# Kernel tuning notes

Hardware: AMD Instinct MI355X
Metric: run time of the kernel (lower is better)

The kernel has to match this reference:

```python
import jax, jax.numpy as jnp
import numpy as np

HEAD_DIM = 64
EMBED_DIM = 1024


def setup_inputs() -> dict:
    key = jax.random.key(0)
    k0, k1, k2, k3, k4, k5, k6 = jax.random.split(key, 7)
    B, T = 4, 2048
    s = 1.0 / np.sqrt(EMBED_DIM)
    return {
        "inputs": jax.random.normal(k0, (B, T, EMBED_DIM), dtype=jnp.float32),
        "Wq": jax.random.uniform(k1, (HEAD_DIM, EMBED_DIM), jnp.float32, -s, s),
        "bq": jax.random.uniform(k2, (HEAD_DIM,), jnp.float32, -s, s),
        "Wk": jax.random.uniform(k3, (HEAD_DIM, EMBED_DIM), jnp.float32, -s, s),
        "bk": jax.random.uniform(k4, (HEAD_DIM,), jnp.float32, -s, s),
        "Wv": jax.random.uniform(k5, (HEAD_DIM, EMBED_DIM), jnp.float32, -s, s),
        "bv": jax.random.uniform(k6, (HEAD_DIM,), jnp.float32, -s, s),
    }


def reference(inputs, Wq, bq, Wk, bk, Wv, bv):
    # inputs: [B, T, E]
    q = jnp.einsum("bte,he->bth", inputs, Wq) + bq  # [B, T, H]
    k = jnp.einsum("bte,he->bth", inputs, Wk) + bk
    v = jnp.einsum("bte,he->bth", inputs, Wv) + bv
    scores = jnp.einsum("bth,bsh->bts", q, k)  # [B, T, T]
    T = scores.shape[-1]
    causal = jnp.tril(jnp.ones((T, T), dtype=bool))  # True = keep
    scores = jnp.where(causal, scores, -jnp.inf)
    weights = jax.nn.softmax(scores / jnp.sqrt(jnp.float32(HEAD_DIM)), axis=-1)
    # dropout is identity in eval mode
    return jnp.einsum("bts,bsh->bth", weights, v)
```

## Files before the change

### kernel.cpp

```cpp
#include <hip/hip_runtime.h>
#include <hip/hip_bf16.h>

#define BATCH 4
#define SEQ   2048
#define EMB   1024
#define HD    64
#define BT    (BATCH * SEQ)
#define XS_STRIDE 1040

#define QSCALE 0.18033688011112042f

typedef __attribute__((ext_vector_type(8))) short bf16x8;
typedef __attribute__((ext_vector_type(4))) float f32x4;

__device__ __forceinline__ ushort f2bf(float f) {
    unsigned u = __float_as_uint(f);
    return (ushort)((u + 0x7FFFu + ((u >> 16) & 1u)) >> 16);
}

__global__ __launch_bounds__(256) void prep(
    const float* __restrict__ Wq, const float* __restrict__ bq,
    const float* __restrict__ Wk, const float* __restrict__ bk,
    const float* __restrict__ Wv, const float* __restrict__ bv,
    ushort* __restrict__ Wf, float* __restrict__ bb)
{
    const int fid = (int)blockIdx.x * 256 + (int)threadIdx.x;
    const int kc   = fid / 768;
    const int rem  = fid - kc * 768;
    const int sub  = rem >> 6;
    const int lane = rem & 63;
    const int row  = (sub & 3) * 16 + (lane & 15);
    const int e0   = kc * 32 + (lane >> 4) * 8;
    const float* W = (sub < 4) ? Wq : ((sub < 8) ? Wk : Wv);
    const float4 a0 = *(const float4*)(W + (size_t)row * EMB + e0);
    const float4 a1 = *(const float4*)(W + (size_t)row * EMB + e0 + 4);
    bf16x8 w;
    w[0] = (short)f2bf(a0.x); w[1] = (short)f2bf(a0.y);
    w[2] = (short)f2bf(a0.z); w[3] = (short)f2bf(a0.w);
    w[4] = (short)f2bf(a1.x); w[5] = (short)f2bf(a1.y);
    w[6] = (short)f2bf(a1.z); w[7] = (short)f2bf(a1.w);
    *(bf16x8*)(Wf + (size_t)fid * 8) = w;
    if (blockIdx.x == 0 && threadIdx.x < 192) {
        const int i = (int)threadIdx.x;
        const float* B = (i < 64) ? bq : ((i < 128) ? bk : bv);
        bb[i] = B[i & 63];
    }
}

__global__ __launch_bounds__(256) void qkv_gemm(
    const float* __restrict__ x, const ushort* __restrict__ Wf,
    const float* __restrict__ bb,
    ushort* __restrict__ Qf, ushort* __restrict__ Kf, ushort* __restrict__ Vf)
{
    const int t0   = (int)blockIdx.x * 16;
    const int tid  = (int)threadIdx.x;
    const int wv   = tid >> 6;
    const int lane = tid & 63;
    const int col  = lane & 15, quad = lane >> 4;

    __shared__ ushort xs[16][XS_STRIDE];

    #pragma unroll 4
    for (int it = 0; it < 16; ++it) {
        const int idx = it * 256 + tid;
        const int row = idx >> 8, c4 = idx & 255;
        const float4 v = *(const float4*)(x + (size_t)(t0 + row) * EMB + c4 * 4);
        ushort4 pk;
        pk.x = f2bf(v.x); pk.y = f2bf(v.y); pk.z = f2bf(v.z); pk.w = f2bf(v.w);
        *(ushort4*)&xs[row][c4 * 4] = pk;
    }
    __syncthreads();

    f32x4 acc[3];
    #pragma unroll
    for (int s = 0; s < 3; ++s) acc[s] = (f32x4){0.f, 0.f, 0.f, 0.f};
    const int sub0 = wv * 3;

    #pragma unroll 4
    for (int kc = 0; kc < 32; ++kc) {
        const bf16x8 a = *(const bf16x8*)&xs[col][kc * 32 + quad * 8];
        #pragma unroll
        for (int s = 0; s < 3; ++s) {
            const bf16x8 w = *(const bf16x8*)(Wf + ((size_t)(kc * 12 + sub0 + s) * 64 + lane) * 8);
            acc[s] = __builtin_amdgcn_mfma_f32_16x16x32_bf16(a, w, acc[s], 0, 0, 0);
        }
    }

    const int b  = t0 >> 11;
    const int qt = (t0 >> 4) & 127;
    const int sg = t0 + quad * 4;
    const int itk = (sg & (SEQ - 1)) >> 6;
    #pragma unroll
    for (int s = 0; s < 3; ++s) {
        const int sub  = sub0 + s;
        const int hrow = sub * 16 + col;
        const float bias = bb[hrow];
        if (sub < 4) {
            const int h = hrow;
            const int f = h >> 5, qd = (h >> 3) & 3, j = h & 7;
            ushort* base = Qf + (((size_t)(b * 128 + qt) * 2 + f) * 64 + qd * 16 + quad * 4) * 8 + j;
            #pragma unroll
            for (int i = 0; i < 4; ++i)
                base[i * 8] = f2bf((acc[s][i] + bias) * QSCALE);
        } else if (sub < 8) {
            const int h = hrow - 64;
            const int f = h >> 5, qd = (h >> 3) & 3, j = h & 7;
            const size_t frag = ((size_t)(b * 32 + itk) * 4 + ((sg >> 4) & 3)) * 2 + f;
            ushort* base = Kf + frag * 512 + ((size_t)((sg & 15) + 16 * qd)) * 8 + j;
            #pragma unroll
            for (int i = 0; i < 4; ++i)
                base[i * 8] = f2bf(acc[s][i] + bias);
        } else {
            const int h = hrow - 128;
            const int k0 = sg & 63;
            const int f = k0 >> 5, qd = (k0 >> 3) & 3, j0 = k0 & 7;
            const size_t frag = ((size_t)(b * 32 + itk) * 4 + (h >> 4)) * 2 + f;
            ushort4 pk;
            pk.x = f2bf(acc[s][0] + bias); pk.y = f2bf(acc[s][1] + bias);
            pk.z = f2bf(acc[s][2] + bias); pk.w = f2bf(acc[s][3] + bias);
            *(ushort4*)(Vf + frag * 512 + ((size_t)((h & 15) + 16 * qd)) * 8 + j0) = pk;
        }
    }
}

__global__ __launch_bounds__(64, 3) void attn_part(
    const ushort* __restrict__ Qf, const ushort* __restrict__ Kf,
    const ushort* __restrict__ Vf,
    float* __restrict__ pm, float* __restrict__ pl, float* __restrict__ pO)
{
    const int idx  = (int)blockIdx.x;
    const int j    = idx & 7;
    const int rest = idx >> 3;
    const int b    = rest & 3;
    const int tile = 127 - (rest >> 2);
    const int t0   = tile * 16;
    const int nt   = (tile >> 2) + 1;
    const int lane = (int)threadIdx.x;
    const int col  = lane & 15, quad = lane >> 4;

    const ushort* Qb = Qf + ((size_t)(b * 128 + tile) * 2) * 512;
    const bf16x8 aq0 = *(const bf16x8*)(Qb + (size_t)lane * 8);
    const bf16x8 aq1 = *(const bf16x8*)(Qb + 512 + (size_t)lane * 8);

    float m_r[4], l_r[4];
    f32x4 o[4];
    #pragma unroll
    for (int i = 0; i < 4; ++i) { m_r[i] = -1e30f; l_r[i] = 0.f; o[i] = (f32x4){0.f,0.f,0.f,0.f}; }

    __shared__ ushort pt[16][80];

    bf16x8 kc[4][2];
    {
        const ushort* Kt = Kf + ((size_t)(b * 32 + j) * 8) * 512;
        #pragma unroll
        for (int sub = 0; sub < 4; ++sub) {
            kc[sub][0] = *(const bf16x8*)(Kt + (size_t)(sub * 2 + 0) * 512 + (size_t)lane * 8);
            kc[sub][1] = *(const bf16x8*)(Kt + (size_t)(sub * 2 + 1) * 512 + (size_t)lane * 8);
        }
    }

    for (int it = j; it < nt; it += 8) {
        const int s0 = it * 64;

        f32x4 sc[4];
        #pragma unroll
        for (int sub = 0; sub < 4; ++sub) {
            f32x4 z = {0.f, 0.f, 0.f, 0.f};
            z = __builtin_amdgcn_mfma_f32_16x16x32_bf16(aq0, kc[sub][0], z, 0, 0, 0);
            z = __builtin_amdgcn_mfma_f32_16x16x32_bf16(aq1, kc[sub][1], z, 0, 0, 0);
            sc[sub] = z;
        }

        const int itn = (it + 8 < nt) ? it + 8 : it;
        bf16x8 kn[4][2], vf[4][2];
        {
            const ushort* Kt = Kf + ((size_t)(b * 32 + itn) * 8) * 512;
            const ushort* Vt = Vf + ((size_t)(b * 32 + it) * 8) * 512;
            #pragma unroll
            for (int sub = 0; sub < 4; ++sub) {
                kn[sub][0] = *(const bf16x8*)(Kt + (size_t)(sub * 2 + 0) * 512 + (size_t)lane * 8);
                kn[sub][1] = *(const bf16x8*)(Kt + (size_t)(sub * 2 + 1) * 512 + (size_t)lane * 8);
                vf[sub][0] = *(const bf16x8*)(Vt + (size_t)(sub * 2 + 0) * 512 + (size_t)lane * 8);
                vf[sub][1] = *(const bf16x8*)(Vt + (size_t)(sub * 2 + 1) * 512 + (size_t)lane * 8);
            }
        }

        if (it == nt - 1) {
            #pragma unroll
            for (int sub = 0; sub < 4; ++sub)
                #pragma unroll
                for (int i = 0; i < 4; ++i) {
                    const int s = s0 + sub * 16 + col, t = t0 + quad * 4 + i;
                    if (s > t) sc[sub][i] = -1e30f;
                }
        }

        float mx[4], alpha[4], ps[4];
        #pragma unroll
        for (int i = 0; i < 4; ++i)
            mx[i] = fmaxf(fmaxf(sc[0][i], sc[1][i]), fmaxf(sc[2][i], sc[3][i]));
        #pragma unroll
        for (int d = 1; d < 16; d <<= 1)
            #pragma unroll
            for (int i = 0; i < 4; ++i) mx[i] = fmaxf(mx[i], __shfl_xor(mx[i], d, 64));
        #pragma unroll
        for (int i = 0; i < 4; ++i) {
            const float nm = fmaxf(m_r[i], mx[i]);
            alpha[i] = exp2f(m_r[i] - nm);
            m_r[i] = nm;
            ps[i] = 0.f;
        }
        #pragma unroll
        for (int sub = 0; sub < 4; ++sub)
            #pragma unroll
            for (int i = 0; i < 4; ++i) {
                const float p = exp2f(sc[sub][i] - m_r[i]);
                ps[i] += p;
                pt[quad * 4 + i][sub * 16 + col] = f2bf(p);
            }
        #pragma unroll
        for (int d = 1; d < 16; d <<= 1)
            #pragma unroll
            for (int i = 0; i < 4; ++i) ps[i] += __shfl_xor(ps[i], d, 64);
        #pragma unroll
        for (int i = 0; i < 4; ++i) l_r[i] = l_r[i] * alpha[i] + ps[i];
        #pragma unroll
        for (int sub = 0; sub < 4; ++sub)
            #pragma unroll
            for (int i = 0; i < 4; ++i) o[sub][i] *= alpha[i];

        __asm__ volatile("s_waitcnt lgkmcnt(0)" ::: "memory");
        const bf16x8 ap0 = *(const bf16x8*)&pt[col][quad * 8];
        const bf16x8 ap1 = *(const bf16x8*)&pt[col][32 + quad * 8];

        #pragma unroll
        for (int sub = 0; sub < 4; ++sub) {
            o[sub] = __builtin_amdgcn_mfma_f32_16x16x32_bf16(ap0, vf[sub][0], o[sub], 0, 0, 0);
            o[sub] = __builtin_amdgcn_mfma_f32_16x16x32_bf16(ap1, vf[sub][1], o[sub], 0, 0, 0);
        }

        #pragma unroll
        for (int sub = 0; sub < 4; ++sub) { kc[sub][0] = kn[sub][0]; kc[sub][1] = kn[sub][1]; }
    }

    const size_t base = ((size_t)(b * 128 + tile)) * 8 + j;
    float* Op = pO + base * 1024;
    #pragma unroll
    for (int sub = 0; sub < 4; ++sub)
        #pragma unroll
        for (int i = 0; i < 4; ++i)
            Op[(quad * 4 + i) * 64 + sub * 16 + col] = o[sub][i];
    if (col == 0) {
        #pragma unroll
        for (int i = 0; i < 4; ++i) {
            pm[base * 16 + quad * 4 + i] = m_r[i];
            pl[base * 16 + quad * 4 + i] = l_r[i];
        }
    }
}

__global__ __launch_bounds__(256) void attn_merge(
    const float* __restrict__ pm, const float* __restrict__ pl,
    const float* __restrict__ pO, float* __restrict__ out)
{
    const int blk = (int)blockIdx.x;
    const int b = blk >> 7, t0 = (blk & 127) * 16;
    const int tid = (int)threadIdx.x;
    const int row = tid >> 4, c0 = (tid & 15) * 4;
    const size_t base = (size_t)blk * 8;

    float mj[8];
    float ms = -1e30f;
    #pragma unroll
    for (int j = 0; j < 8; ++j) {
        mj[j] = pm[(base + j) * 16 + row];
        ms = fmaxf(ms, mj[j]);
    }
    float ls = 0.f;
    float4 r = {0.f, 0.f, 0.f, 0.f};
    #pragma unroll
    for (int j = 0; j < 8; ++j) {
        const float w = exp2f(mj[j] - ms);
        ls += w * pl[(base + j) * 16 + row];
        const float4 O = *(const float4*)&pO[(base + j) * 1024 + row * 64 + c0];
        r.x += w * O.x; r.y += w * O.y; r.z += w * O.z; r.w += w * O.w;
    }
    const float rinv = 1.0f / ls;
    float4 res = {r.x * rinv, r.y * rinv, r.z * rinv, r.w * rinv};
    *(float4*)(out + ((size_t)b * SEQ + t0 + row) * HD + c0) = res;
}

extern "C" void kernel_launch(void* const* d_in, const int* in_sizes, int n_in,
                              void* d_out, int out_size, void* d_ws, size_t ws_size,
                              hipStream_t stream)
{
    const float* x  = (const float*)d_in[0];
    const float* Wq = (const float*)d_in[1];
    const float* bq = (const float*)d_in[2];
    const float* Wk = (const float*)d_in[3];
    const float* bk = (const float*)d_in[4];
    const float* Wv = (const float*)d_in[5];
    const float* bv = (const float*)d_in[6];
    float* out = (float*)d_out;

    char* ws = (char*)d_ws;
    ushort* Wf  = (ushort*)(ws);
    float*  bb  = (float*)(ws + 0x60000);
    ushort* Qfb = (ushort*)(ws + 0x61000);
    ushort* Kfb = (ushort*)(ws + 0x161000);
    ushort* Vfb = (ushort*)(ws + 0x261000);
    float*  pmb = (float*)(ws + 0x400000);
    float*  plb = (float*)(ws + 0x440000);
    float*  pOb = (float*)(ws + 0x480000);

    prep<<<96, 256, 0, stream>>>(Wq, bq, Wk, bk, Wv, bv, Wf, bb);
    qkv_gemm<<<BT / 16, 256, 0, stream>>>(x, Wf, bb, Qfb, Kfb, Vfb);
    attn_part<<<4096, 64, 0, stream>>>(Qfb, Kfb, Vfb, pmb, plb, pOb);
    attn_merge<<<512, 256, 0, stream>>>(pmb, plb, pOb, out);
}
```

Before: 116.1 us.

## Fuse split-K merge into attention kernel via last-block atomic counter

Removes the separate attn_merge launch. Each attention partial block bumps a per-tile atomic counter, and the last of the 8 split blocks for a tile combines the partial max, sum and O values and writes the output. Counters are zeroed in the prep kernel. This saves one kernel launch and its tail, at the cost of fences, an atomic per block, and a serialized merge done by a single 64-lane wave per tile.

```diff
diff --git a/kernel.cpp b/kernel.cpp
--- a/kernel.cpp
+++ b/kernel.cpp
@@ -22,7 +22,7 @@
     const float* __restrict__ Wq, const float* __restrict__ bq,
     const float* __restrict__ Wk, const float* __restrict__ bk,
     const float* __restrict__ Wv, const float* __restrict__ bv,
-    ushort* __restrict__ Wf, float* __restrict__ bb)
+    ushort* __restrict__ Wf, float* __restrict__ bb, int* __restrict__ cnt)
 {
     const int fid = (int)blockIdx.x * 256 + (int)threadIdx.x;
     const int kc   = fid / 768;
@@ -45,6 +45,8 @@
         const float* B = (i < 64) ? bq : ((i < 128) ? bk : bv);
         bb[i] = B[i & 63];
     }
+    if (blockIdx.x < 2)
+        cnt[(int)blockIdx.x * 256 + (int)threadIdx.x] = 0;
 }
 
 __global__ __launch_bounds__(256) void qkv_gemm(
@@ -126,7 +128,8 @@
 __global__ __launch_bounds__(64, 3) void attn_part(
     const ushort* __restrict__ Qf, const ushort* __restrict__ Kf,
     const ushort* __restrict__ Vf,
-    float* __restrict__ pm, float* __restrict__ pl, float* __restrict__ pO)
+    float* __restrict__ pm, float* __restrict__ pl, float* __restrict__ pO,
+    int* __restrict__ cnt, float* __restrict__ out)
 {
     const int idx  = (int)blockIdx.x;
     const int j    = idx & 7;
@@ -257,37 +260,46 @@
             pl[base * 16 + quad * 4 + i] = l_r[i];
         }
     }
-}
-
-__global__ __launch_bounds__(256) void attn_merge(
-    const float* __restrict__ pm, const float* __restrict__ pl,
-    const float* __restrict__ pO, float* __restrict__ out)
-{
-    const int blk = (int)blockIdx.x;
-    const int b = blk >> 7, t0 = (blk & 127) * 16;
-    const int tid = (int)threadIdx.x;
-    const int row = tid >> 4, c0 = (tid & 15) * 4;
-    const size_t base = (size_t)blk * 8;
-
-    float mj[8];
-    float ms = -1e30f;
-    #pragma unroll
-    for (int j = 0; j < 8; ++j) {
-        mj[j] = pm[(base + j) * 16 + row];
-        ms = fmaxf(ms, mj[j]);
-    }
-    float ls = 0.f;
-    float4 r = {0.f, 0.f, 0.f, 0.f};
-    #pragma unroll
-    for (int j = 0; j < 8; ++j) {
-        const float w = exp2f(mj[j] - ms);
-        ls += w * pl[(base + j) * 16 + row];
-        const float4 O = *(const float4*)&pO[(base + j) * 1024 + row * 64 + c0];
-        r.x += w * O.x; r.y += w * O.y; r.z += w * O.z; r.w += w * O.w;
-    }
-    const float rinv = 1.0f / ls;
-    float4 res = {r.x * rinv, r.y * rinv, r.z * rinv, r.w * rinv};
-    *(float4*)(out + ((size_t)b * SEQ + t0 + row) * HD + c0) = res;
+
+    __threadfence();
+    int prev = 0;
+    if (lane == 0)
+        prev = __hip_atomic_fetch_add(&cnt[b * 128 + tile], 1,
+                                      __ATOMIC_ACQ_REL, __HIP_MEMORY_SCOPE_AGENT);
+    prev = __shfl(prev, 0, 64);
+    if (prev == 7) {
+        __threadfence();
+        const int row = lane >> 2;
+        const size_t mbase = ((size_t)(b * 128 + tile)) * 8;
+        float mj[8];
+        float ms = -1e30f;
+        #pragma unroll
+        for (int k = 0; k < 8; ++k) {
+            mj[k] = pm[(mbase + k) * 16 + row];
+            ms = fmaxf(ms, mj[k]);
+        }
+        float wk[8];
+        float ls = 0.f;
+        #pragma unroll
+        for (int k = 0; k < 8; ++k) {
+            wk[k] = exp2f(mj[k] - ms);
+            ls += wk[k] * pl[(mbase + k) * 16 + row];
+        }
+        const float rinv = 1.0f / ls;
+        #pragma unroll
+        for (int g = 0; g < 4; ++g) {
+            const int c0 = (lane & 3) * 16 + g * 4;
+            float4 r = {0.f, 0.f, 0.f, 0.f};
+            #pragma unroll
+            for (int k = 0; k < 8; ++k) {
+                const float4 O = *(const float4*)&pO[(mbase + k) * 1024 + row * 64 + c0];
+                r.x += wk[k] * O.x; r.y += wk[k] * O.y;
+                r.z += wk[k] * O.z; r.w += wk[k] * O.w;
+            }
+            float4 res = {r.x * rinv, r.y * rinv, r.z * rinv, r.w * rinv};
+            *(float4*)(out + ((size_t)b * SEQ + t0 + row) * HD + c0) = res;
+        }
+    }
 }
 
 extern "C" void kernel_launch(void* const* d_in, const int* in_sizes, int n_in,
@@ -306,6 +318,7 @@
     char* ws = (char*)d_ws;
     ushort* Wf  = (ushort*)(ws);
     float*  bb  = (float*)(ws + 0x60000);
+    int*    cnt = (int*)(ws + 0x60800);
     ushort* Qfb = (ushort*)(ws + 0x61000);
     ushort* Kfb = (ushort*)(ws + 0x161000);
     ushort* Vfb = (ushort*)(ws + 0x261000);
@@ -313,8 +326,7 @@
     float*  plb = (float*)(ws + 0x440000);
     float*  pOb = (float*)(ws + 0x480000);
 
-    prep<<<96, 256, 0, stream>>>(Wq, bq, Wk, bk, Wv, bv, Wf, bb);
+    prep<<<96, 256, 0, stream>>>(Wq, bq, Wk, bk, Wv, bv, Wf, bb, cnt);
     qkv_gemm<<<BT / 16, 256, 0, stream>>>(x, Wf, bb, Qfb, Kfb, Vfb);
-    attn_part<<<4096, 64, 0, stream>>>(Qfb, Kfb, Vfb, pmb, plb, pOb);
-    attn_merge<<<512, 256, 0, stream>>>(pmb, plb, pOb, out);
-}
+    attn_part<<<4096, 64, 0, stream>>>(Qfb, Kfb, Vfb, pmb, plb, pOb, cnt, out);
+}
```

Result: slower. 362.9 us (+212.5%).
